# Optimization experiments

Hardware: AMD Instinct MI355X
Metric: run time of the kernel (lower is better)

Reference implementation:

```python
import jax, jax.numpy as jnp
import numpy as np

EMBED_DIM = 1024
NUM_HEADS = 16
HEAD_DIM = EMBED_DIM // NUM_HEADS


def setup_inputs() -> dict:
    key = jax.random.key(0)
    ks = jax.random.split(key, 7)
    B, S, D = 2, 2048, EMBED_DIM
    scale = 1.0 / np.sqrt(D)
    return {
        "query": jax.random.normal(ks[0], (B, S, D), dtype=jnp.float32),
        "key": jax.random.normal(ks[1], (B, S, D), dtype=jnp.float32),
        "value": jax.random.normal(ks[2], (B, S, D), dtype=jnp.float32),
        "W_qkv": jax.random.normal(ks[3], (D, 3 * D), dtype=jnp.float32) * scale,
        "b_qkv": jnp.zeros((3 * D,), dtype=jnp.float32),
        "W_out": jax.random.normal(ks[4], (D, D), dtype=jnp.float32) * scale,
        "b_out": jnp.zeros((D,), dtype=jnp.float32),
    }


def reference(query, key, value, W_qkv, b_qkv, W_out, b_out):
    # NOTE: the original torch forward ignores `key` and `value` — q,k,v all
    # come from qkv_proj(query). We keep them as args for signature fidelity.
    B, S, D = query.shape
    H, hd = NUM_HEADS, HEAD_DIM
    scale = hd ** -0.5

    qkv = query @ W_qkv + b_qkv                      # [B, S, 3D]
    qkv = qkv.reshape(B, S, 3, H, hd)
    q = jnp.transpose(qkv[:, :, 0], (0, 2, 1, 3))    # [B, H, S, hd]
    k = jnp.transpose(qkv[:, :, 1], (0, 2, 1, 3))
    v = jnp.transpose(qkv[:, :, 2], (0, 2, 1, 3))

    scores = jnp.einsum("bhsd,bhtd->bhst", q, k) * scale  # [B, H, S, S]
    attn = jax.nn.softmax(scores, axis=-1)
    out = jnp.einsum("bhst,bhtd->bhsd", attn, v)           # [B, H, S, hd]
    out = jnp.transpose(out, (0, 2, 1, 3)).reshape(B, S, D)
    return out @ W_out + b_out
```

## Files before the change

### kernel.cpp

```cpp
#include <hip/hip_runtime.h>
#include <stdint.h>

#define DEV static __device__ __forceinline__

typedef __attribute__((ext_vector_type(4))) float f32x4;
typedef __attribute__((ext_vector_type(16))) float f32x16;
typedef __attribute__((ext_vector_type(8))) short bf16x8;
typedef bf16x8 __attribute__((may_alias)) bf16x8_a;
typedef __attribute__((ext_vector_type(2))) unsigned int u32x2;
typedef u32x2 __attribute__((may_alias)) u32x2_a;

DEV unsigned short f2bf(float f) {
  union { float f; unsigned int u; } v; v.f = f;
  return (unsigned short)((v.u + 0x7FFFu + ((v.u >> 16) & 1u)) >> 16);
}

DEV float bf2f(unsigned short s) {
  union { unsigned int u; float f; } v; v.u = ((unsigned int)s) << 16;
  return v.f;
}

DEV float fast_exp2(float x) {
  float r;
  asm("v_exp_f32 %0, %1" : "=v"(r) : "v"(x));
  return r;
}

DEV unsigned int pktrunc(float lo, float hi) {
  union { float f; unsigned int u; } a, b; a.f = lo; b.f = hi;
  return __builtin_amdgcn_perm(b.u, a.u, 0x07060302u);
}

DEV void gload_lds16(const void* g, void* l) {
  __builtin_amdgcn_global_load_lds(
      (const __attribute__((address_space(1))) unsigned int*)g,
      (__attribute__((address_space(3))) unsigned int*)l, 16, 0, 0);
}

DEV void transpose_body(const float* __restrict__ in, unsigned short* __restrict__ out,
                        int R, int C, int bx, int by, int t, float (*tile)[33]) {
  const int r = t >> 3, c4 = (t & 7) << 2;
  const int tr = by << 5, tc = bx << 5;
  const float4 v = *(const float4*)(in + (size_t)(tr + r) * C + tc + c4);
  tile[r][c4] = v.x; tile[r][c4 + 1] = v.y; tile[r][c4 + 2] = v.z; tile[r][c4 + 3] = v.w;
  __syncthreads();
  ushort4 o;
  o.x = f2bf(tile[c4][r]); o.y = f2bf(tile[c4 + 1][r]);
  o.z = f2bf(tile[c4 + 2][r]); o.w = f2bf(tile[c4 + 3][r]);
  *(ushort4*)(out + (size_t)(tc + r) * R + tr + c4) = o;
}

__global__ __launch_bounds__(256) void prep_k(const float4* __restrict__ q4,
                                              ushort4* __restrict__ Xb,
                                              const float* __restrict__ Wqkv,
                                              unsigned short* __restrict__ WqkvT,
                                              const float* __restrict__ Wout,
                                              unsigned short* __restrict__ WoutT) {
  __shared__ float tile[32][33];
  const int t = threadIdx.x, bid = blockIdx.x;
  if (bid < 4096) {
    const int i = bid * 256 + t;
    float4 f = q4[i];
    ushort4 o; o.x = f2bf(f.x); o.y = f2bf(f.y); o.z = f2bf(f.z); o.w = f2bf(f.w);
    Xb[i] = o;
  } else if (bid < 4096 + 3072) {
    const int id = bid - 4096;
    transpose_body(Wqkv, WqkvT, 1024, 3072, id % 96, id / 96, t, tile);
  } else {
    const int id = bid - 4096 - 3072;
    transpose_body(Wout, WoutT, 1024, 1024, id & 31, id >> 5, t, tile);
  }
}

template <int EPI, int BN, int TM>
__global__ __launch_bounds__(256, 6) void gemm_bt(const unsigned short* __restrict__ A,
                                                  const unsigned short* __restrict__ BT,
                                                  const float* __restrict__ bias,
                                                  float* __restrict__ Cout,
                                                  unsigned short* __restrict__ q_buf,
                                                  unsigned short* __restrict__ k_buf,
                                                  unsigned short* __restrict__ vT_buf,
                                                  int M, int N, int K) {
  constexpr int NWM = (TM == 64) ? 2 : ((BN == 128) ? 2 : 4);
  constexpr int NWN = 4 / NWM;
  constexpr int MI = TM / NWM / 16;
  constexpr int MW = MI * 16;
  __shared__ unsigned short As[2][TM * 32];
  __shared__ unsigned short Bs[2][BN * 32];
  const int t = threadIdx.x, w = t >> 6, l = t & 63;
  const int wm = (NWM == 2) ? (w >> 1) : w;
  const int wn = (NWN == 2) ? (w & 1) : 0;
  const int lg = l >> 4, ln = l & 15;

  const int xcd = blockIdx.x & 7, jb = blockIdx.x >> 3;
  const int per_xcd = (M / TM) >> 3;
  const int m0 = (xcd * per_xcd + (jb % per_xcd)) * TM;
  const int n0 = (jb / per_xcd) * BN;

  const int srow = t >> 2;
  const int schunk = (t & 3) ^ ((t >> 3) & 3);
  const int dchunk = t & 3;

  f32x4 acc[MI][4] = {};

#define STAGE_G(buf, k0)                                                                              \
  do {                                                                                                \
    gload_lds16(A + (size_t)(m0 + srow) * K + (k0) + schunk * 8, &As[buf][srow * 32 + dchunk * 8]);   \
    if (TM == 128)                                                                                    \
      gload_lds16(A + (size_t)(m0 + srow + 64) * K + (k0) + schunk * 8,                               \
                  &As[buf][(srow + 64) * 32 + dchunk * 8]);                                           \
    gload_lds16(BT + (size_t)(n0 + srow) * K + (k0) + schunk * 8, &Bs[buf][srow * 32 + dchunk * 8]);  \
    if (BN == 128)                                                                                    \
      gload_lds16(BT + (size_t)(n0 + srow + 64) * K + (k0) + schunk * 8,                              \
                  &Bs[buf][(srow + 64) * 32 + dchunk * 8]);                                           \
  } while (0)

  STAGE_G(0, 0);
  __syncthreads();

  const int rchunk = (lg ^ ((ln >> 1) & 3)) << 3;
  const int nit = K >> 5;
  for (int it = 0; it < nit; ++it) {
    const int buf = it & 1;
    if (it + 1 < nit) STAGE_G(buf ^ 1, (it + 1) * 32);

    bf16x8 af[MI], bfr[4];
#pragma unroll
    for (int mi = 0; mi < MI; ++mi)
      af[mi] = *(const bf16x8_a*)&As[buf][(wm * MW + mi * 16 + ln) * 32 + rchunk];
#pragma unroll
    for (int ni = 0; ni < 4; ++ni)
      bfr[ni] = *(const bf16x8_a*)&Bs[buf][(wn * 64 + ni * 16 + ln) * 32 + rchunk];
#pragma unroll
    for (int mi = 0; mi < MI; ++mi)
#pragma unroll
      for (int ni = 0; ni < 4; ++ni)
        acc[mi][ni] = __builtin_amdgcn_mfma_f32_16x16x32_bf16(af[mi], bfr[ni], acc[mi][ni], 0, 0, 0);

    __syncthreads();
  }
#undef STAGE_G

#pragma unroll
  for (int ni = 0; ni < 4; ++ni) {
    const int c = n0 + wn * 64 + ni * 16 + ln;
    const float bv = bias[c];
    if (EPI == 1) {
      const int which = c >> 10;
      const int h = (c >> 6) & 15;
      const int d = c & 63;
#pragma unroll
      for (int mi = 0; mi < MI; ++mi) {
        const int mrow = m0 + wm * MW + mi * 16 + lg * 4;
        const int b = mrow >> 11, s = mrow & 2047;
        const size_t bh = (size_t)(b * 16 + h);
        f32x4 v = acc[mi][ni];
        if (which == 0) {
          const float QSCALE = 0.125f * 1.44269504088896340736f;
          unsigned short* dst = q_buf + (bh * 2048 + s) * 64 + d;
#pragma unroll
          for (int r = 0; r < 4; ++r) dst[(size_t)r * 64] = f2bf((v[r] + bv) * QSCALE);
        } else if (which == 1) {
          unsigned short* dst = k_buf + (bh * 2048 + s) * 64 + d;
#pragma unroll
          for (int r = 0; r < 4; ++r) dst[(size_t)r * 64] = f2bf(v[r] + bv);
        } else {
          const int sp = (s & ~12) | ((s & 4) << 1) | ((s & 8) >> 1);
          unsigned short* dst = vT_buf + (bh * 64 + d) * 2048 + sp;
          ushort4 o4;
          o4.x = f2bf(v[0] + bv); o4.y = f2bf(v[1] + bv); o4.z = f2bf(v[2] + bv); o4.w = f2bf(v[3] + bv);
          *(ushort4*)dst = o4;
        }
      }
    } else {
#pragma unroll
      for (int mi = 0; mi < MI; ++mi) {
        const int mrow = m0 + wm * MW + mi * 16 + lg * 4;
        f32x4 v = acc[mi][ni];
#pragma unroll
        for (int r = 0; r < 4; ++r) Cout[(size_t)(mrow + r) * N + c] = v[r] + bv;
      }
    }
  }
}

template <int SPLIT>
__global__ __launch_bounds__(256, 4) void attn_k(const unsigned short* __restrict__ Qb,
                                                 const unsigned short* __restrict__ Kb,
                                                 const unsigned short* __restrict__ Vt,
                                                 unsigned short* __restrict__ AO,
                                                 unsigned short* __restrict__ Opart,
                                                 float* __restrict__ lpart) {
  constexpr int NT = 32 / SPLIT;
  const float SHIFT = -16.0f;
  __shared__ unsigned short Ks[2][64 * 64];
  __shared__ unsigned short Vs[2][64 * 64];

  const int t = threadIdx.x, w = t >> 6, l = t & 63;
  const int l31 = l & 31, lh = l >> 5;
  const int xcd = blockIdx.x & 7, idx = blockIdx.x >> 3;
  const int bh = xcd * 4 + (idx & 3);
  const int qt = (SPLIT == 2) ? ((idx >> 2) & 15) : (idx >> 2);
  const int half = (SPLIT == 2) ? (idx >> 6) : 0;
  const int b = bh >> 4, h = bh & 15;
  const unsigned short* Q = Qb + (size_t)bh * 2048 * 64;
  const unsigned short* K = Kb + (size_t)bh * 2048 * 64 + (size_t)half * NT * 64 * 64;
  const unsigned short* V = Vt + (size_t)bh * 64 * 2048 + half * NT * 64;
  const int qbase = qt * 128 + w * 32;

  const int srow = t >> 3;
  const int scol = ((t & 7) ^ (srow & 7)) << 3;
  const int dcol = (t & 7) << 3;

  bf16x8 qf[4];
#pragma unroll
  for (int kd = 0; kd < 4; ++kd)
    qf[kd] = *(const bf16x8_a*)(Q + (size_t)(qbase + l31) * 64 + kd * 16 + lh * 8);

  bf16x8 ones;
#pragma unroll
  for (int i = 0; i < 8; ++i) ones[i] = (short)0x3F80;

  f32x16 o32[2] = {};
  f32x16 lsum = {};

  {
    gload_lds16(K + (size_t)srow * 64 + scol,        &Ks[0][srow * 64 + dcol]);
    gload_lds16(K + (size_t)(srow + 32) * 64 + scol, &Ks[0][(srow + 32) * 64 + dcol]);
    gload_lds16(V + (size_t)srow * 2048 + scol,        &Vs[0][srow * 64 + dcol]);
    gload_lds16(V + (size_t)(srow + 32) * 2048 + scol, &Vs[0][(srow + 32) * 64 + dcol]);
  }
  __syncthreads();

  for (int tk = 0; tk < NT; ++tk) {
    const int cur = tk & 1;
    if (tk < NT - 1) {
      const int k1 = (tk + 1) * 64;
      const unsigned short* Kg = K + (size_t)k1 * 64;
      const unsigned short* Vg = V + k1;
      gload_lds16(Kg + (size_t)srow * 64 + scol,        &Ks[cur ^ 1][srow * 64 + dcol]);
      gload_lds16(Kg + (size_t)(srow + 32) * 64 + scol, &Ks[cur ^ 1][(srow + 32) * 64 + dcol]);
      gload_lds16(Vg + (size_t)srow * 2048 + scol,        &Vs[cur ^ 1][srow * 64 + dcol]);
      gload_lds16(Vg + (size_t)(srow + 32) * 2048 + scol, &Vs[cur ^ 1][(srow + 32) * 64 + dcol]);
    }

    f32x16 sa[2] = {};
#pragma unroll
    for (int m2 = 0; m2 < 2; ++m2)
#pragma unroll
      for (int kd = 0; kd < 4; ++kd) {
        const bf16x8 kf = *(const bf16x8_a*)
            &Ks[cur][(m2 * 32 + l31) * 64 + (((kd * 2 + lh) ^ (l & 7)) << 3)];
        sa[m2] = __builtin_amdgcn_mfma_f32_32x32x16_bf16(kf, qf[kd], sa[m2], 0, 0, 0);
      }

    bf16x8 vf0[4];
#pragma unroll
    for (int ksI = 0; ksI < 4; ++ksI)
      vf0[ksI] = *(const bf16x8_a*)&Vs[cur][l31 * 64 + (((ksI * 2 + lh) ^ (l & 7)) << 3)];

    unsigned int pk[2][8];
#pragma unroll
    for (int m2 = 0; m2 < 2; ++m2) {
      float p[16];
#pragma unroll
      for (int r = 0; r < 16; ++r) p[r] = fast_exp2(sa[m2][r] + SHIFT);
#pragma unroll
      for (int u = 0; u < 8; ++u) pk[m2][u] = pktrunc(p[2 * u], p[2 * u + 1]);
    }

    union { unsigned int u[4]; bf16x8 v; } pa[4];
#pragma unroll
    for (int m2 = 0; m2 < 2; ++m2)
#pragma unroll
      for (int ks2 = 0; ks2 < 2; ++ks2) {
        const int ksI = m2 * 2 + ks2;
        pa[ksI].u[0] = pk[m2][ks2 * 4 + 0];
        pa[ksI].u[1] = pk[m2][ks2 * 4 + 1];
        pa[ksI].u[2] = pk[m2][ks2 * 4 + 2];
        pa[ksI].u[3] = pk[m2][ks2 * 4 + 3];
      }
#pragma unroll
    for (int ksI = 0; ksI < 4; ++ksI) {
      const bf16x8 vf1 = *(const bf16x8_a*)
          &Vs[cur][(32 + l31) * 64 + (((ksI * 2 + lh) ^ (l & 7)) << 3)];
      o32[0] = __builtin_amdgcn_mfma_f32_32x32x16_bf16(pa[ksI].v, vf0[ksI], o32[0], 0, 0, 0);
      lsum   = __builtin_amdgcn_mfma_f32_32x32x16_bf16(pa[ksI].v, ones,     lsum,   0, 0, 0);
      o32[1] = __builtin_amdgcn_mfma_f32_32x32x16_bf16(pa[ksI].v, vf1,      o32[1], 0, 0, 0);
    }

    __syncthreads();
  }

  if (SPLIT == 2) {
    const size_t pbase = ((size_t)(half * 32 + bh) * 2048 + qbase);
#pragma unroll
    for (int nb = 0; nb < 2; ++nb)
#pragma unroll
      for (int r = 0; r < 16; ++r) {
        const int qrow = (r & 3) + 8 * (r >> 2) + 4 * lh;
        Opart[(pbase + qrow) * 64 + nb * 32 + l31] = f2bf(o32[nb][r]);
      }
    if (l31 == 0) {
#pragma unroll
      for (int r = 0; r < 16; ++r)
        lpart[pbase + (r & 3) + 8 * (r >> 2) + 4 * lh] = lsum[r];
    }
  } else {
#pragma unroll
    for (int nb = 0; nb < 2; ++nb)
#pragma unroll
      for (int r = 0; r < 16; ++r) {
        const int qrow = (r & 3) + 8 * (r >> 2) + 4 * lh;
        const size_t row = (size_t)b * 2048 + qbase + qrow;
        AO[row * 1024 + h * 64 + nb * 32 + l31] = f2bf(o32[nb][r] / lsum[r]);
      }
  }
}

__global__ __launch_bounds__(256) void merge_k(const unsigned short* __restrict__ Opart,
                                               const float* __restrict__ lpart,
                                               unsigned short* __restrict__ AO) {
  const int u = blockIdx.x * 256 + threadIdx.x;
  const int c8 = u & 7, s = (u >> 3) & 2047, bh = u >> 14;
  const int b = bh >> 4, h = bh & 15;
  const size_t r0 = (size_t)bh * 2048 + s;
  const size_t r1 = (size_t)(32 + bh) * 2048 + s;
  const bf16x8 a0 = *(const bf16x8_a*)(Opart + r0 * 64 + c8 * 8);
  const bf16x8 a1 = *(const bf16x8_a*)(Opart + r1 * 64 + c8 * 8);
  const float inv = 1.0f / (lpart[r0] + lpart[r1]);
  bf16x8 oo;
#pragma unroll
  for (int i = 0; i < 8; ++i)
    oo[i] = (short)f2bf((bf2f((unsigned short)a0[i]) + bf2f((unsigned short)a1[i])) * inv);
  *(bf16x8_a*)(AO + ((size_t)b * 2048 + s) * 1024 + h * 64 + c8 * 8) = oo;
}

extern "C" void kernel_launch(void* const* d_in, const int* in_sizes, int n_in,
                              void* d_out, int out_size, void* d_ws, size_t ws_size,
                              hipStream_t stream) {
  const float* query = (const float*)d_in[0];
  const float* W_qkv = (const float*)d_in[3];
  const float* b_qkv = (const float*)d_in[4];
  const float* W_out = (const float*)d_in[5];
  const float* b_out = (const float*)d_in[6];
  float* out = (float*)d_out;
  char* ws = (char*)d_ws;

  unsigned short* Xb    = (unsigned short*)(ws);
  unsigned short* WqkvT = (unsigned short*)(ws + 8388608);
  unsigned short* WoutT = (unsigned short*)(ws + 14680064);
  unsigned short* qb    = (unsigned short*)(ws + 16777216);
  unsigned short* kb    = (unsigned short*)(ws + 25165824);
  unsigned short* vT    = (unsigned short*)(ws + 33554432);
  unsigned short* Opart = (unsigned short*)(ws + 41943040);
  float*          lpart = (float*)(ws + 58720256);
  const bool split2 = ws_size >= 59244544;
  unsigned short* AO    = Xb;

  prep_k<<<8192, 256, 0, stream>>>((const float4*)query, (ushort4*)Xb,
                                   W_qkv, WqkvT, W_out, WoutT);
  gemm_bt<1, 128, 64><<<1536, 256, 0, stream>>>(Xb, WqkvT, b_qkv, nullptr, qb, kb, vT,
                                                4096, 3072, 1024);
  if (split2) {
    attn_k<2><<<1024, 256, 0, stream>>>(qb, kb, vT, nullptr, Opart, lpart);
    merge_k<<<2048, 256, 0, stream>>>(Opart, lpart, AO);
  } else {
    attn_k<1><<<512, 256, 0, stream>>>(qb, kb, vT, AO, nullptr, nullptr);
  }
  gemm_bt<0, 64, 128><<<512, 256, 0, stream>>>(AO, WoutT, b_out, out, nullptr, nullptr, nullptr,
                                               4096, 1024, 1024);
}
```

Measured before the change: 127.1 us.

## Restructure GEMM to 128-row tiles with single-buffered K=64 stages

The bf16 GEMM kernel is rewritten to use a fixed 128-row M tile and a 64-wide K step. It uses a single LDS buffer with an 8-chunk XOR swizzle, where it previously used a double-buffered 32-wide K pipeline. The QKV projection now launches 768 blocks of 128x128 tiles instead of 1536 blocks of 64x128, so each loaded tile gets more reuse. The cost is that global loads no longer overlap with MFMA work inside a block, and occupancy drops to a launch bound of 3 blocks per CU, so the kernel relies on other resident blocks to hide latency.

```diff
diff --git a/kernel.cpp b/kernel.cpp
--- a/kernel.cpp
+++ b/kernel.cpp
@@ -72,8 +72,8 @@
   }
 }
 
-template <int EPI, int BN, int TM>
-__global__ __launch_bounds__(256, 6) void gemm_bt(const unsigned short* __restrict__ A,
+template <int EPI, int BN>
+__global__ __launch_bounds__(256, 3) void gemm_bt(const unsigned short* __restrict__ A,
                                                   const unsigned short* __restrict__ BT,
                                                   const float* __restrict__ bias,
                                                   float* __restrict__ Cout,
@@ -81,77 +81,69 @@
                                                   unsigned short* __restrict__ k_buf,
                                                   unsigned short* __restrict__ vT_buf,
                                                   int M, int N, int K) {
-  constexpr int NWM = (TM == 64) ? 2 : ((BN == 128) ? 2 : 4);
-  constexpr int NWN = 4 / NWM;
-  constexpr int MI = TM / NWM / 16;
-  constexpr int MW = MI * 16;
-  __shared__ unsigned short As[2][TM * 32];
-  __shared__ unsigned short Bs[2][BN * 32];
+  constexpr int NI = BN / 32;
+  constexpr int NW = BN / 2;
+  __shared__ unsigned short As[128 * 64];
+  __shared__ unsigned short Bs[BN * 64];
   const int t = threadIdx.x, w = t >> 6, l = t & 63;
-  const int wm = (NWM == 2) ? (w >> 1) : w;
-  const int wn = (NWN == 2) ? (w & 1) : 0;
+  const int wm = w >> 1, wn = w & 1;
   const int lg = l >> 4, ln = l & 15;
 
   const int xcd = blockIdx.x & 7, jb = blockIdx.x >> 3;
-  const int per_xcd = (M / TM) >> 3;
-  const int m0 = (xcd * per_xcd + (jb % per_xcd)) * TM;
-  const int n0 = (jb / per_xcd) * BN;
-
-  const int srow = t >> 2;
-  const int schunk = (t & 3) ^ ((t >> 3) & 3);
-  const int dchunk = t & 3;
-
-  f32x4 acc[MI][4] = {};
-
-#define STAGE_G(buf, k0)                                                                              \
-  do {                                                                                                \
-    gload_lds16(A + (size_t)(m0 + srow) * K + (k0) + schunk * 8, &As[buf][srow * 32 + dchunk * 8]);   \
-    if (TM == 128)                                                                                    \
-      gload_lds16(A + (size_t)(m0 + srow + 64) * K + (k0) + schunk * 8,                               \
-                  &As[buf][(srow + 64) * 32 + dchunk * 8]);                                           \
-    gload_lds16(BT + (size_t)(n0 + srow) * K + (k0) + schunk * 8, &Bs[buf][srow * 32 + dchunk * 8]);  \
-    if (BN == 128)                                                                                    \
-      gload_lds16(BT + (size_t)(n0 + srow + 64) * K + (k0) + schunk * 8,                              \
-                  &Bs[buf][(srow + 64) * 32 + dchunk * 8]);                                           \
+  const int m0 = (xcd * 4 + (jb & 3)) * 128;
+  const int n0 = (jb >> 2) * BN;
+
+  const int sch = (t & 7) ^ ((t >> 3) & 7);
+
+  f32x4 acc[4][NI] = {};
+
+#define STAGE97(k0)                                                                      \
+  do {                                                                                   \
+    _Pragma("unroll")                                                                    \
+    for (int j = 0; j < 4; ++j)                                                          \
+      gload_lds16(A + (size_t)(m0 + (t >> 3) + j * 32) * K + (k0) + sch * 8,             \
+                  &As[((t >> 3) + j * 32) * 64 + (t & 7) * 8]);                          \
+    _Pragma("unroll")                                                                    \
+    for (int j = 0; j < BN / 32; ++j)                                                    \
+      gload_lds16(BT + (size_t)(n0 + (t >> 3) + j * 32) * K + (k0) + sch * 8,            \
+                  &Bs[((t >> 3) + j * 32) * 64 + (t & 7) * 8]);                          \
   } while (0)
 
-  STAGE_G(0, 0);
-  __syncthreads();
-
-  const int rchunk = (lg ^ ((ln >> 1) & 3)) << 3;
-  const int nit = K >> 5;
-  for (int it = 0; it < nit; ++it) {
-    const int buf = it & 1;
-    if (it + 1 < nit) STAGE_G(buf ^ 1, (it + 1) * 32);
-
-    bf16x8 af[MI], bfr[4];
-#pragma unroll
-    for (int mi = 0; mi < MI; ++mi)
-      af[mi] = *(const bf16x8_a*)&As[buf][(wm * MW + mi * 16 + ln) * 32 + rchunk];
-#pragma unroll
-    for (int ni = 0; ni < 4; ++ni)
-      bfr[ni] = *(const bf16x8_a*)&Bs[buf][(wn * 64 + ni * 16 + ln) * 32 + rchunk];
-#pragma unroll
-    for (int mi = 0; mi < MI; ++mi)
-#pragma unroll
-      for (int ni = 0; ni < 4; ++ni)
-        acc[mi][ni] = __builtin_amdgcn_mfma_f32_16x16x32_bf16(af[mi], bfr[ni], acc[mi][ni], 0, 0, 0);
-
+  for (int kt = 0; kt < K; kt += 64) {
+    STAGE97(kt);
     __syncthreads();
-  }
-#undef STAGE_G
-
-#pragma unroll
-  for (int ni = 0; ni < 4; ++ni) {
-    const int c = n0 + wn * 64 + ni * 16 + ln;
+#pragma unroll
+    for (int kk = 0; kk < 2; ++kk) {
+      bf16x8 af[4], bfr[NI];
+#pragma unroll
+      for (int mi = 0; mi < 4; ++mi)
+        af[mi] = *(const bf16x8_a*)&As[(wm * 64 + mi * 16 + ln) * 64 +
+                                       (((kk * 4 + lg) ^ (ln & 7)) << 3)];
+#pragma unroll
+      for (int ni = 0; ni < NI; ++ni)
+        bfr[ni] = *(const bf16x8_a*)&Bs[(wn * NW + ni * 16 + ln) * 64 +
+                                        (((kk * 4 + lg) ^ (ln & 7)) << 3)];
+#pragma unroll
+      for (int mi = 0; mi < 4; ++mi)
+#pragma unroll
+        for (int ni = 0; ni < NI; ++ni)
+          acc[mi][ni] = __builtin_amdgcn_mfma_f32_16x16x32_bf16(af[mi], bfr[ni], acc[mi][ni], 0, 0, 0);
+    }
+    __syncthreads();
+  }
+#undef STAGE97
+
+#pragma unroll
+  for (int ni = 0; ni < NI; ++ni) {
+    const int c = n0 + wn * NW + ni * 16 + ln;
     const float bv = bias[c];
     if (EPI == 1) {
       const int which = c >> 10;
       const int h = (c >> 6) & 15;
       const int d = c & 63;
 #pragma unroll
-      for (int mi = 0; mi < MI; ++mi) {
-        const int mrow = m0 + wm * MW + mi * 16 + lg * 4;
+      for (int mi = 0; mi < 4; ++mi) {
+        const int mrow = m0 + wm * 64 + mi * 16 + lg * 4;
         const int b = mrow >> 11, s = mrow & 2047;
         const size_t bh = (size_t)(b * 16 + h);
         f32x4 v = acc[mi][ni];
@@ -174,8 +166,8 @@
       }
     } else {
 #pragma unroll
-      for (int mi = 0; mi < MI; ++mi) {
-        const int mrow = m0 + wm * MW + mi * 16 + lg * 4;
+      for (int mi = 0; mi < 4; ++mi) {
+        const int mrow = m0 + wm * 64 + mi * 16 + lg * 4;
         f32x4 v = acc[mi][ni];
 #pragma unroll
         for (int r = 0; r < 4; ++r) Cout[(size_t)(mrow + r) * N + c] = v[r] + bv;
@@ -360,14 +352,14 @@
 
   prep_k<<<8192, 256, 0, stream>>>((const float4*)query, (ushort4*)Xb,
                                    W_qkv, WqkvT, W_out, WoutT);
-  gemm_bt<1, 128, 64><<<1536, 256, 0, stream>>>(Xb, WqkvT, b_qkv, nullptr, qb, kb, vT,
-                                                4096, 3072, 1024);
+  gemm_bt<1, 128><<<768, 256, 0, stream>>>(Xb, WqkvT, b_qkv, nullptr, qb, kb, vT,
+                                           4096, 3072, 1024);
   if (split2) {
     attn_k<2><<<1024, 256, 0, stream>>>(qb, kb, vT, nullptr, Opart, lpart);
     merge_k<<<2048, 256, 0, stream>>>(Opart, lpart, AO);
   } else {
     attn_k<1><<<512, 256, 0, stream>>>(qb, kb, vT, AO, nullptr, nullptr);
   }
-  gemm_bt<0, 64, 128><<<512, 256, 0, stream>>>(AO, WoutT, b_out, out, nullptr, nullptr, nullptr,
-                                               4096, 1024, 1024);
-}
+  gemm_bt<0, 64><<<512, 256, 0, stream>>>(AO, WoutT, b_out, out, nullptr, nullptr, nullptr,
+                                          4096, 1024, 1024);
+}
```

Result: faster. 113.8 us (-10.5%).
